# Kernel tuning notes

Hardware: AMD Instinct MI355X
Metric: run time of the kernel (lower is better)

## Reference

```python
import jax, jax.numpy as jnp
import numpy as np

P, M, DG, F, H, DH = 2000, 150, 2000, 256, 4, 64
N1, N2 = P + M, P + DG          # adj1 nodes (patient+med), adj2 nodes (patient+diag)
E1, E2, EGP, EGM = 137600, 256000, 64000, 4800
GNN_LAYERS = 2
SA_HID = 128


def setup_inputs() -> dict:
    key = jax.random.key(0)
    ks = jax.random.split(key, 32)
    ri = lambda k, n, hi: jax.random.randint(k, (n,), 0, hi, dtype=jnp.int32)
    rn = lambda k, shape, scale: (jax.random.normal(k, shape, dtype=jnp.float32) * scale)
    inp = {
        'adj1_rows': ri(ks[0], E1, N1), 'adj1_cols': ri(ks[1], E1, N1),
        'adj1_vals': jax.random.uniform(ks[2], (E1,), dtype=jnp.float32),
        'adj2_rows': ri(ks[3], E2, N2), 'adj2_cols': ri(ks[4], E2, N2),
        'adj2_vals': jax.random.uniform(ks[5], (E2,), dtype=jnp.float32),
        'g0_src': ri(ks[6], EGP, P), 'g0_dst': ri(ks[7], EGP, P),
        'g1_src': ri(ks[8], EGP, P), 'g1_dst': ri(ks[9], EGP, P),
        'g2_src': ri(ks[10], EGM, M), 'g2_dst': ri(ks[11], EGM, M),
        'g3_src': ri(ks[12], EGM, M), 'g3_dst': ri(ks[13], EGM, M),
        'keepRate': 1,
        # learned parameters (xavier-ish scales)
        'pEmbed': rn(ks[14], (P, F), 0.05),
        'mEmbed': rn(ks[15], (M, F), 0.05),
        'dEmbed': rn(ks[16], (DG, F), 0.05),
        'gat_W': rn(ks[17], (4, F, H * DH), (2.0 / (F + H * DH)) ** 0.5),
        'gat_al': rn(ks[18], (4, H, DH), 0.1),
        'gat_ar': rn(ks[19], (4, H, DH), 0.1),
        'gat_b': jnp.zeros((4, H * DH), dtype=jnp.float32),
        'sa_W1': rn(ks[20], (H * DH, SA_HID), (2.0 / (H * DH + SA_HID)) ** 0.5),
        'sa_b1': jnp.zeros((SA_HID,), dtype=jnp.float32),
        'sa_W2': rn(ks[21], (SA_HID, 1), 0.1),
        'out_W': rn(ks[22], (2 * F, M), (2.0 / (2 * F + M)) ** 0.5),
        'out_b': jnp.zeros((M,), dtype=jnp.float32),
    }
    return inp


def _spmm(rows, cols, vals, x, n):
    # sparse adj @ x via gather + segment_sum
    return jax.ops.segment_sum(vals[:, None] * x[cols], rows, num_segments=n)


def _seg_softmax(e, seg, n):
    m = jax.ops.segment_max(e, seg, num_segments=n)          # [n, H]
    ex = jnp.exp(e - m[seg])
    s = jax.ops.segment_sum(ex, seg, num_segments=n)
    return ex / (s[seg] + 1e-9)


def _gat(h, W, al, ar, b, src, dst, n):
    # DGL GATConv, feat/attn dropout = 0, negative_slope = 0.2, activation = elu
    feat = (h @ W).reshape(n, H, DH)                          # [n, H, DH]
    el = (feat * al[None]).sum(-1)                            # [n, H]
    er = (feat * ar[None]).sum(-1)
    e = jax.nn.leaky_relu(el[src] + er[dst], negative_slope=0.2)  # [E, H]
    alpha = _seg_softmax(e, dst, n)                           # softmax over in-edges per dst
    out = jax.ops.segment_sum(alpha[:, :, None] * feat[src], dst, num_segments=n)
    out = out + b.reshape(1, H, DH)
    return jax.nn.elu(out).reshape(n, H * DH)


def _sem_att(z, W1, b1, W2):
    # z: [N, K, F]; shared projection; beta over K meta-paths
    w = (jnp.tanh(z @ W1 + b1) @ W2).mean(0)                  # [K, 1]
    beta = jax.nn.softmax(w, axis=0)                          # [K, 1]
    return (beta[None] * z).sum(1)                            # [N, F]


def reference(adj1_rows, adj1_cols, adj1_vals, adj2_rows, adj2_cols, adj2_vals,
              g0_src, g0_dst, g1_src, g1_dst, g2_src, g2_dst, g3_src, g3_dst,
              keepRate, pEmbed, mEmbed, dEmbed, gat_W, gat_al, gat_ar, gat_b,
              sa_W1, sa_b1, sa_W2, out_W, out_b):
    embeds1 = jnp.concatenate([pEmbed, mEmbed], axis=0)       # [N1, F]
    embeds2 = jnp.concatenate([pEmbed, dEmbed], axis=0)       # [N2, F]
    lat1, lat2 = embeds1, embeds2
    acc1 = jnp.zeros_like(embeds1)
    acc2 = jnp.zeros_like(embeds2)
    for _ in range(GNN_LAYERS):
        lat1 = jax.nn.leaky_relu(_spmm(adj1_rows, adj1_cols, adj1_vals, lat1, N1), negative_slope=0.5)
        lat2 = jax.nn.leaky_relu(_spmm(adj2_rows, adj2_cols, adj2_vals, lat2, N2), negative_slope=0.5)
        acc1 = acc1 + lat1
        acc2 = acc2 + lat2
    p1, m_gcn = acc1[:P], acc1[P:]
    p2, d_gcn = acc2[:P], acc2[P:]

    e0 = _gat(p1, gat_W[0], gat_al[0], gat_ar[0], gat_b[0], g0_src, g0_dst, P)
    e1 = _gat(p2, gat_W[1], gat_al[1], gat_ar[1], gat_b[1], g1_src, g1_dst, P)
    e2 = _gat(m_gcn, gat_W[2], gat_al[2], gat_ar[2], gat_b[2], g2_src, g2_dst, M)
    e3 = _gat(m_gcn, gat_W[3], gat_al[3], gat_ar[3], gat_b[3], g3_src, g3_dst, M)

    patient = _sem_att(jnp.stack([e0, e1], axis=1), sa_W1, sa_b1, sa_W2)  # [P, F]
    med = _sem_att(jnp.stack([e2, e3], axis=1), sa_W1, sa_b1, sa_W2)      # [M, F]

    # broadcasted pairwise concat -> ReLU -> Linear -> sum over pairing axis
    pm = jnp.concatenate([
        jnp.broadcast_to(patient[:, None, :], (P, M, F)),
        jnp.broadcast_to(med[None, :, :], (P, M, F)),
    ], axis=-1).reshape(P * M, 2 * F)
    simi = (jax.nn.relu(pm) @ out_W + out_b).reshape(P, M, M)
    simi_pm = simi.sum(axis=1)                                # [P, M]
    return (simi_pm, d_gcn, med, m_gcn, patient)
```

## Files before the change

### kernel.cpp

```cpp
#include <hip/hip_runtime.h>
#include <hip/hip_fp16.h>
#include <cmath>
#include <cstdint>

constexpr int P  = 2000, M = 150, DG = 2000, F = 256, H = 4, DH = 64;
constexpr int N1 = P + M;
constexpr int N2 = P + DG;
constexpr int E1 = 137600, E2 = 256000, EGP = 64000, EGM = 4800;
constexpr int SA_HID = 128;

constexpr int HO1 = E1, HO2 = E1 + E2, HO3 = HO2 + EGP, HO4 = HO3 + EGP,
              HO5 = HO4 + EGM, HOE = HO5 + EGM;

constexpr int CAP_A = 160;
constexpr int CAP_G = 96;
constexpr int OVF_CAP = 4096;

constexpr int CPAD = 16;

__device__ __forceinline__ float4 h4_to_f4(const __half* p) {
  union { ushort4 u4; __half2 h2[2]; } u;
  u.u4 = *(const ushort4*)p;
  float2 lo = __half22float2(u.h2[0]);
  float2 hi = __half22float2(u.h2[1]);
  return make_float4(lo.x, lo.y, hi.x, hi.y);
}
__device__ __forceinline__ void f4_to_h4(__half* p, float4 v) {
  union { ushort4 u4; __half2 h2[2]; } u;
  u.h2[0] = __float22half2_rn(make_float2(v.x, v.y));
  u.h2[1] = __float22half2_rn(make_float2(v.z, v.w));
  *(ushort4*)p = u.u4;
}

constexpr int CAST_CH = (P * F + M * F + DG * F) / 8;

__global__ __launch_bounds__(256) void k_build(
    const int* __restrict__ a1r, const int* __restrict__ a1c, const float* __restrict__ a1v,
    const int* __restrict__ a2r, const int* __restrict__ a2c, const float* __restrict__ a2v,
    const int* __restrict__ d0, const int* __restrict__ s0,
    const int* __restrict__ d1, const int* __restrict__ s1,
    const int* __restrict__ d2, const int* __restrict__ s2,
    const int* __restrict__ d3, const int* __restrict__ s3,
    int* cur1, uint2* ell1, int* cur2, uint2* ell2,
    int* cu0, unsigned* eg0, int* cu1, unsigned* eg1,
    int* cu2, unsigned* eg2, int* cu3, unsigned* eg3,
    int* __restrict__ ovf_n, int4* __restrict__ ovf,
    const float* __restrict__ pEf, const float* __restrict__ mEf,
    const float* __restrict__ dEf,
    __half* __restrict__ pEh, __half* __restrict__ mEh, __half* __restrict__ dEh) {
  int tid = blockIdx.x * 256 + threadIdx.x;
  int T = gridDim.x * 256;
  int seg[4], row[4]; unsigned p0[4], p1[4];
#pragma unroll
  for (int u = 0; u < 4; ++u) {
    int i = tid + u * T;
    seg[u] = -1;
    if (i < HOE) {
      if (i < HO1)      { seg[u] = 0; row[u] = a1r[i]; p0[u] = (unsigned)a1c[i]; p1[u] = __float_as_uint(a1v[i]); }
      else if (i < HO2) { int j = i - HO1; seg[u] = 1; row[u] = a2r[j]; p0[u] = (unsigned)a2c[j]; p1[u] = __float_as_uint(a2v[j]); }
      else if (i < HO3) { int j = i - HO2; seg[u] = 2; row[u] = d0[j]; p0[u] = (unsigned)s0[j]; }
      else if (i < HO4) { int j = i - HO3; seg[u] = 3; row[u] = d1[j]; p0[u] = (unsigned)s1[j]; }
      else if (i < HO5) { int j = i - HO4; seg[u] = 4; row[u] = d2[j]; p0[u] = (unsigned)s2[j]; }
      else              { int j = i - HO5; seg[u] = 5; row[u] = d3[j]; p0[u] = (unsigned)s3[j]; }
    }
  }
#pragma unroll
  for (int u = 0; u < 4; ++u) {
    int r = row[u];
    switch (seg[u]) {
      case 0: { int slot = atomicAdd(&cur1[(size_t)r * CPAD], 1);
        if (slot < CAP_A) ell1[(size_t)r * CAP_A + slot] = make_uint2(p0[u], p1[u]);
        else { int o = atomicAdd(&ovf_n[0], 1); if (o < OVF_CAP) ovf[0 * OVF_CAP + o] = make_int4(r, (int)p0[u], (int)p1[u], 0); } } break;
      case 1: { int slot = atomicAdd(&cur2[(size_t)r * CPAD], 1);
        if (slot < CAP_A) ell2[(size_t)r * CAP_A + slot] = make_uint2(p0[u], p1[u]);
        else { int o = atomicAdd(&ovf_n[1], 1); if (o < OVF_CAP) ovf[1 * OVF_CAP + o] = make_int4(r, (int)p0[u], (int)p1[u], 0); } } break;
      case 2: { int slot = atomicAdd(&cu0[(size_t)r * CPAD], 1);
        if (slot < CAP_G) eg0[(size_t)r * CAP_G + slot] = p0[u];
        else { int o = atomicAdd(&ovf_n[2], 1); if (o < OVF_CAP) ovf[2 * OVF_CAP + o] = make_int4(r, (int)p0[u], 0, 0); } } break;
      case 3: { int slot = atomicAdd(&cu1[(size_t)r * CPAD], 1);
        if (slot < CAP_G) eg1[(size_t)r * CAP_G + slot] = p0[u];
        else { int o = atomicAdd(&ovf_n[3], 1); if (o < OVF_CAP) ovf[3 * OVF_CAP + o] = make_int4(r, (int)p0[u], 0, 0); } } break;
      case 4: { int slot = atomicAdd(&cu2[(size_t)r * CPAD], 1);
        if (slot < CAP_G) eg2[(size_t)r * CAP_G + slot] = p0[u];
        else { int o = atomicAdd(&ovf_n[4], 1); if (o < OVF_CAP) ovf[4 * OVF_CAP + o] = make_int4(r, (int)p0[u], 0, 0); } } break;
      case 5: { int slot = atomicAdd(&cu3[(size_t)r * CPAD], 1);
        if (slot < CAP_G) eg3[(size_t)r * CAP_G + slot] = p0[u];
        else { int o = atomicAdd(&ovf_n[5], 1); if (o < OVF_CAP) ovf[5 * OVF_CAP + o] = make_int4(r, (int)p0[u], 0, 0); } } break;
      default: break;
    }
  }
  for (int c = tid; c < CAST_CH; c += T) {
    int j = c * 8;
    const float* src; __half* dst;
    if (j < P * F)              { src = pEf + j;               dst = pEh + j; }
    else if (j < P * F + M * F) { src = mEf + (j - P * F);     dst = mEh + (j - P * F); }
    else                        { src = dEf + (j - P*F - M*F); dst = dEh + (j - P*F - M*F); }
    float4 a = *(const float4*)src, b = *(const float4*)(src + 4);
    f4_to_h4(dst, a);
    f4_to_h4(dst + 4, b);
  }
}

template<int LAYER>
__global__ __launch_bounds__(256) void k_spmm(
    const int* __restrict__ cur1, const uint2* __restrict__ ell1,
    const int* __restrict__ cur2, const uint2* __restrict__ ell2,
    const int* __restrict__ ovf_n, const int4* __restrict__ ovf,
    const __half* __restrict__ pEh, const __half* __restrict__ mEh,
    const __half* __restrict__ dEh,
    float* __restrict__ lat1f, float* __restrict__ lat2f,
    __half* __restrict__ lat1h, __half* __restrict__ lat2h,
    float* __restrict__ acc1, float* __restrict__ acc2,
    float* __restrict__ out_mgcn, float* __restrict__ out_dgcn) {
  int grp = (blockIdx.x * 256 + threadIdx.x) >> 7;
  int lane = threadIdx.x & 63;
  int wh   = (threadIdx.x >> 6) & 1;
  int gl   = threadIdx.x >> 7;
  bool g2 = grp >= N1;
  int row = g2 ? grp - N1 : grp;
  const uint2* pe = (g2 ? ell2 : ell1) + (size_t)row * CAP_A;
  const __half* latinh = g2 ? lat2h : lat1h;
  const __half* tailEh = g2 ? dEh : mEh;
  int deg = (g2 ? cur2 : cur1)[(size_t)row * CPAD];
  int dn = deg < CAP_A ? deg : CAP_A;
  int fo = lane << 2;
  float4 s = {0.f, 0.f, 0.f, 0.f};
  auto fetch = [&](int c) -> float4 {
    const __half* b;
    if (LAYER == 1) b = (c < P) ? (pEh + (size_t)c * F) : (tailEh + (size_t)(c - P) * F);
    else            b = latinh + (size_t)c * F;
    return h4_to_f4(b + fo);
  };
// ... 26 lines not shown
  }
  {
    int gi = g2 ? 1 : 0;
    int on = ovf_n[gi];
    if (on > 0) {
      const int4* ol = ovf + gi * OVF_CAP;
      for (int k = 0; k < on; ++k) {
        int4 e = ol[k];
        if (e.x == row) {
          float v = __int_as_float(e.z);
          float4 a = fetch(e.y);
          s.x += v * a.x; s.y += v * a.y; s.z += v * a.z; s.w += v * a.w;
        }
      }
    }
  }
  float4 l;
  l.x = s.x > 0.f ? s.x : 0.5f * s.x;
  l.y = s.y > 0.f ? s.y : 0.5f * s.y;
  l.z = s.z > 0.f ? s.z : 0.5f * s.z;
  l.w = s.w > 0.f ? s.w : 0.5f * s.w;
  if (LAYER == 1) {
    *(float4*)((g2 ? lat2f : lat1f) + (size_t)row * F + fo) = l;
    f4_to_h4((g2 ? lat2h : lat1h) + (size_t)row * F + fo, l);
  } else {
    const float* latf = g2 ? lat2f : lat1f;
    float4 b = *(const float4*)(latf + (size_t)row * F + fo);
    float4 a = {b.x + l.x, b.y + l.y, b.z + l.z, b.w + l.w};
    *(float4*)((g2 ? acc2 : acc1) + (size_t)row * F + fo) = a;
    if (row >= P)
      *(float4*)((g2 ? out_dgcn : out_mgcn) + (size_t)(row - P) * F + fo) = a;
  }
}

constexpr int FR  = 8;
constexpr int NB0 = (P + FR - 1) / FR;
constexpr int NB2 = (M + FR - 1) / FR;
constexpr int FEAT_BLOCKS = 2 * NB0 + 2 * NB2;

__global__ __launch_bounds__(256) void k_gat_feat_all(
    const float* __restrict__ acc1, const float* __restrict__ acc2,
    const float* __restrict__ gat_W, const float* __restrict__ gat_al,
    const float* __restrict__ gat_ar,
    __half* __restrict__ f0, __half* __restrict__ f1,
    __half* __restrict__ f2, __half* __restrict__ f3,
    float* __restrict__ el, float* __restrict__ er) {
  int b = blockIdx.x;
  int g, rb, n; const float* h; __half* fout;
  if (b < NB0)            { g = 0; rb = b;              n = P; h = acc1; fout = f0; }
  else if (b < 2 * NB0)   { g = 1; rb = b - NB0;        n = P; h = acc2; fout = f1; }
  else if (b < 2*NB0+NB2) { g = 2; rb = b - 2 * NB0;    n = M; h = acc1 + (size_t)P * F; fout = f2; }
  else                    { g = 3; rb = b - 2*NB0 - NB2; n = M; h = acc1 + (size_t)P * F; fout = f3; }
  int elo = (g == 0) ? 0 : (g == 1) ? P * H : (g == 2) ? 2 * P * H : (2 * P + M) * H;
  const float* W = gat_W + (size_t)g * F * F;
  __shared__ float hs[FR][F];
  int t = threadIdx.x;
  int r0 = rb * FR;
  for (int q = t; q < FR * 64; q += 256) {
    int r = q >> 6, ln = q & 63;
    int row = r0 + r;
    float4 v = {0.f, 0.f, 0.f, 0.f};
    if (row < n) v = *(const float4*)(h + (size_t)row * F + (ln << 2));
    *(float4*)&hs[r][ln << 2] = v;
  }
  __syncthreads();
  float acc[FR];
#pragma unroll
  for (int r = 0; r < FR; ++r) acc[r] = 0.f;
  for (int k = 0; k < F; k += 4) {
    float w0 = W[(size_t)k * F + t],       w1 = W[(size_t)(k + 1) * F + t],
          w2 = W[(size_t)(k + 2) * F + t], w3 = W[(size_t)(k + 3) * F + t];
// ... 107 lines not shown
  __shared__ float4 pacc[2][64];
  __shared__ float  pss[2][64];
  if (wh == 1) { pacc[gl][lane] = acc; pss[gl][lane] = ssum; }
  __syncthreads();
  if (wh == 1) return;
  {
    float4 pa = pacc[gl][lane];
    acc.x += pa.x; acc.y += pa.y; acc.z += pa.z; acc.w += pa.w;
    ssum += pss[gl][lane];
  }
  if (on > 0) {
    for (int k = 0; k < on; ++k) {
      int4 e = ol[k];
      if (e.x == row) {
        float a = elb[e.y * H + head] + erv; a = a > 0.f ? a : 0.2f * a;
        float x0 = expf(a - mx);
        float4 q0 = h4_to_f4(feat + (size_t)e.y * F + fo);
        ssum += x0;
        acc.x += x0 * q0.x; acc.y += x0 * q0.y; acc.z += x0 * q0.z; acc.w += x0 * q0.w;
      }
    }
  }
  float inv = 1.f / (ssum + 1e-9f);
  const float* bb = gat_b + g * F + fo;
  float4 v = {acc.x * inv + bb[0], acc.y * inv + bb[1],
              acc.z * inv + bb[2], acc.w * inv + bb[3]};
  v.x = v.x > 0.f ? v.x : expm1f(v.x);
  v.y = v.y > 0.f ? v.y : expm1f(v.y);
  v.z = v.z > 0.f ? v.z : expm1f(v.z);
  v.w = v.w > 0.f ? v.w : expm1f(v.w);
  *(float4*)(out + (size_t)row * F + fo) = v;
}

constexpr int SR  = 4;
constexpr int SB0 = (P + SR - 1) / SR;
constexpr int SB2 = (M + SR - 1) / SR;
constexpr int SEM_BLOCKS = 2 * SB0 + 2 * SB2;

__global__ __launch_bounds__(128) void k_sem_w_all(
    const float* __restrict__ e0, const float* __restrict__ e1,
    const float* __restrict__ e2, const float* __restrict__ e3,
    const float* __restrict__ W1, const float* __restrict__ b1,
    const float* __restrict__ W2, float* __restrict__ w) {
  int b = blockIdx.x;
  int zid, rb, n; const float* z;
  if (b < SB0)            { zid = 0; rb = b;             n = P; z = e0; }
  else if (b < 2 * SB0)   { zid = 1; rb = b - SB0;       n = P; z = e1; }
  else if (b < 2*SB0+SB2) { zid = 2; rb = b - 2 * SB0;   n = M; z = e2; }
  else                    { zid = 3; rb = b - 2*SB0-SB2; n = M; z = e3; }
  __shared__ float zs[SR][F];
  int t = threadIdx.x;
  int r0 = rb * SR;
  for (int q = t; q < SR * 64; q += 128) {
    int r = q >> 6, ln = q & 63;
    int row = r0 + r;
    float4 v = {0.f, 0.f, 0.f, 0.f};
    if (row < n) v = *(const float4*)(z + (size_t)row * F + (ln << 2));
    *(float4*)&zs[r][ln << 2] = v;
  }
  __syncthreads();
  float hid[SR];
#pragma unroll
  for (int r = 0; r < SR; ++r) hid[r] = b1[t];
  for (int k = 0; k < F; k += 4) {
    float w0 = W1[(size_t)k * SA_HID + t],       w1 = W1[(size_t)(k + 1) * SA_HID + t],
          w2 = W1[(size_t)(k + 2) * SA_HID + t], w3 = W1[(size_t)(k + 3) * SA_HID + t];
#pragma unroll
    for (int r = 0; r < SR; ++r) {
      float4 z4 = *(const float4*)&zs[r][k];
      hid[r] += z4.x * w0 + z4.y * w1 + z4.z * w2 + z4.w * w3;
    }
// ... 27 lines not shown
    float4 u0 = ((const float4*)e2)[j], u1 = ((const float4*)e3)[j];
    float4 r = {a0 * u0.x + a1 * u1.x, a0 * u0.y + a1 * u1.y,
                a0 * u0.z + a1 * u1.z, a0 * u0.w + a1 * u1.w};
    ((float4*)out_med)[j] = r;
    rs.x += r.x > 0.f ? r.x : 0.f;
    rs.y += r.y > 0.f ? r.y : 0.f;
    rs.z += r.z > 0.f ? r.z : 0.f;
    rs.w += r.w > 0.f ? r.w : 0.f;
  }
  __shared__ float4 sv4[4][64];
  sv4[t >> 6][t & 63] = rs;
  __syncthreads();
  __shared__ float sv[F];
  if (t < 64) {
    float4 a = sv4[0][t], b = sv4[1][t], c = sv4[2][t], d = sv4[3][t];
    sv[t * 4 + 0] = a.x + b.x + c.x + d.x;
    sv[t * 4 + 1] = a.y + b.y + c.y + d.y;
    sv[t * 4 + 2] = a.z + b.z + c.z + d.z;
    sv[t * 4 + 3] = a.w + b.w + c.w + d.w;
  }
  __syncthreads();
  if (t < M) {
    float cc = (float)M * outb[t];
    for (int f = 0; f < F; f += 4) {
      cc += sv[f]     * outW[(size_t)(F + f) * M + t]
          + sv[f + 1] * outW[(size_t)(F + f + 1) * M + t]
          + sv[f + 2] * outW[(size_t)(F + f + 2) * M + t]
          + sv[f + 3] * outW[(size_t)(F + f + 3) * M + t];
    }
    cbuf[t] = cc;
  }
}

constexpr int FIN_R = 4;
__global__ __launch_bounds__(256) void k_final(
    const float* __restrict__ e0, const float* __restrict__ e1,
    const float* __restrict__ w, const float* __restrict__ outW,
    const float* __restrict__ c,
    float* __restrict__ out_pat, float* __restrict__ simi) {
  float m0 = w[0] * (1.f / P), m1 = w[1] * (1.f / P);
  float mxv = fmaxf(m0, m1);
  float a0 = expf(m0 - mxv), a1 = expf(m1 - mxv);
  float sc = 1.f / (a0 + a1);
  a0 *= sc; a1 *= sc;
  __shared__ float psh[FIN_R][F];
  int t = threadIdx.x;
  int r0 = blockIdx.x * FIN_R;
  for (int q = t; q < FIN_R * 64; q += 256) {
    int r = q >> 6, ln = q & 63;
    size_t off = (size_t)(r0 + r) * F + (ln << 2);
    float4 u0 = *(const float4*)(e0 + off), u1 = *(const float4*)(e1 + off);
    float4 v = {a0 * u0.x + a1 * u1.x, a0 * u0.y + a1 * u1.y,
                a0 * u0.z + a1 * u1.z, a0 * u0.w + a1 * u1.w};
    *(float4*)(out_pat + off) = v;
    v.x = v.x > 0.f ? v.x : 0.f; v.y = v.y > 0.f ? v.y : 0.f;
    v.z = v.z > 0.f ? v.z : 0.f; v.w = v.w > 0.f ? v.w : 0.f;
    *(float4*)&psh[r][ln << 2] = v;
  }
  __syncthreads();
  if (t < M) {
    float acc[FIN_R];
#pragma unroll
    for (int r = 0; r < FIN_R; ++r) acc[r] = 0.f;
    for (int f = 0; f < F; f += 4) {
      float w0 = outW[(size_t)f * M + t],       w1 = outW[(size_t)(f + 1) * M + t],
            w2 = outW[(size_t)(f + 2) * M + t], w3 = outW[(size_t)(f + 3) * M + t];
#pragma unroll
// ... 17 lines not shown
  const int*   adj2_rows = (const int*)d_in[3];
  const int*   adj2_cols = (const int*)d_in[4];
  const float* adj2_vals = (const float*)d_in[5];
  const int*   g0_src = (const int*)d_in[6];
  const int*   g0_dst = (const int*)d_in[7];
  const int*   g1_src = (const int*)d_in[8];
  const int*   g1_dst = (const int*)d_in[9];
  const int*   g2_src = (const int*)d_in[10];
  const int*   g2_dst = (const int*)d_in[11];
  const int*   g3_src = (const int*)d_in[12];
  const int*   g3_dst = (const int*)d_in[13];
  const float* pE     = (const float*)d_in[15];
  const float* mE     = (const float*)d_in[16];
  const float* dE     = (const float*)d_in[17];
  const float* gat_W  = (const float*)d_in[18];
  const float* gat_al = (const float*)d_in[19];
  const float* gat_ar = (const float*)d_in[20];
  const float* gat_b  = (const float*)d_in[21];
  const float* sa_W1  = (const float*)d_in[22];
  const float* sa_b1  = (const float*)d_in[23];
  const float* sa_W2  = (const float*)d_in[24];
  const float* out_W  = (const float*)d_in[25];
  const float* out_b  = (const float*)d_in[26];

  int* ip = (int*)d_ws;
  int* cur1 = ip; ip += (size_t)N1 * CPAD;
  int* cur2 = ip; ip += (size_t)N2 * CPAD;
  int* cu0  = ip; ip += (size_t)P * CPAD;
  int* cu1  = ip; ip += (size_t)P * CPAD;
  int* cu2  = ip; ip += (size_t)M * CPAD;
  int* cu3  = ip; ip += (size_t)M * CPAD;
  int* ovf_n = ip; ip += 6;
  float* wbuf = (float*)ip; ip += 4;
  size_t memset_bytes = (size_t)((char*)ip - (char*)d_ws);

  uintptr_t up = ((uintptr_t)ip + 15) & ~(uintptr_t)15;
  int4* ovf = (int4*)up;
  uint2* ell1 = (uint2*)(ovf + 6 * OVF_CAP);
  uint2* ell2 = ell1 + (size_t)N1 * CAP_A;
  unsigned* eg0 = (unsigned*)(ell2 + (size_t)N2 * CAP_A);
  unsigned* eg1 = eg0 + (size_t)P * CAP_G;
  unsigned* eg2 = eg1 + (size_t)P * CAP_G;
  unsigned* eg3 = eg2 + (size_t)M * CAP_G;
  __half* hp = (__half*)(eg3 + (size_t)M * CAP_G);
  __half* pEh   = hp; hp += (size_t)P * F;
  __half* mEh   = hp; hp += (size_t)M * F;
  __half* dEh   = hp; hp += (size_t)DG * F;
  __half* lat1h = hp; hp += (size_t)N1 * F;
  __half* lat2h = hp; hp += (size_t)N2 * F;
  __half* f0h   = hp; hp += (size_t)P * F;
  __half* f1h   = hp; hp += (size_t)P * F;
  __half* f2h   = hp; hp += (size_t)M * F;
  __half* f3h   = hp; hp += (size_t)M * F;
  float* fp = (float*)hp;
  float* lat1f = fp; fp += (size_t)N1 * F;
  float* lat2f = fp; fp += (size_t)N2 * F;
  float* acc1  = fp; fp += (size_t)N1 * F;
  float* acc2  = fp; fp += (size_t)N2 * F;
  float* el    = fp; fp += (size_t)(2 * P + 2 * M) * H;
  float* er    = fp; fp += (size_t)(2 * P + 2 * M) * H;
  float* e0b   = fp; fp += (size_t)P * F;
  float* e1b   = fp; fp += (size_t)P * F;
  float* e2b   = fp; fp += (size_t)M * F;
  float* e3b   = fp; fp += (size_t)M * F;
  float* cbuf  = fp; fp += 256;

  float* out_simi = (float*)d_out;
  float* out_dgcn = out_simi + (size_t)P * M;
  float* out_med  = out_dgcn + (size_t)DG * F;
  float* out_mgcn = out_med  + (size_t)M * F;
  float* out_pat  = out_mgcn + (size_t)M * F;

  hipMemsetAsync(d_ws, 0, memset_bytes, stream);

  int eb = ((HOE + 3) / 4 + 255) / 256;
  k_build<<<eb, 256, 0, stream>>>(adj1_rows, adj1_cols, adj1_vals,
                                  adj2_rows, adj2_cols, adj2_vals,
                                  g0_dst, g0_src, g1_dst, g1_src,
                                  g2_dst, g2_src, g3_dst, g3_src,
                                  cur1, ell1, cur2, ell2,
                                  cu0, eg0, cu1, eg1, cu2, eg2, cu3, eg3,
                                  ovf_n, ovf,
                                  pE, mE, dE, pEh, mEh, dEh);

  int sb = (N1 + N2) / 2;
  k_spmm<1><<<sb, 256, 0, stream>>>(cur1, ell1, cur2, ell2, ovf_n, ovf,
                                    pEh, mEh, dEh, lat1f, lat2f, lat1h, lat2h,
                                    acc1, acc2, out_mgcn, out_dgcn);
  k_spmm<2><<<sb, 256, 0, stream>>>(cur1, ell1, cur2, ell2, ovf_n, ovf,
                                    pEh, mEh, dEh, lat1f, lat2f, lat1h, lat2h,
                                    acc1, acc2, out_mgcn, out_dgcn);

  k_gat_feat_all<<<FEAT_BLOCKS, 256, 0, stream>>>(acc1, acc2, gat_W, gat_al, gat_ar,
                                                  f0h, f1h, f2h, f3h, el, er);
  int ab = (2 * P + 2 * M) / 2;
  k_gat_agg_all<<<ab, 256, 0, stream>>>(cu0, eg0, cu1, eg1, cu2, eg2, cu3, eg3,
                                        ovf_n, ovf, el, er, f0h, f1h, f2h, f3h, gat_b,
                                        e0b, e1b, e2b, e3b);

  k_sem_w_all<<<SEM_BLOCKS, 128, 0, stream>>>(e0b, e1b, e2b, e3b, sa_W1, sa_b1, sa_W2, wbuf);

  k_med_cvec<<<1, 256, 0, stream>>>(e2b, e3b, wbuf, out_W, out_b, out_med, cbuf);

  k_final<<<P / FIN_R, 256, 0, stream>>>(e0b, e1b, wbuf, out_W, cbuf, out_pat, out_simi);
}
```

Baseline: 307.0 us.

## Fuse whole pipeline into one cooperative persistent kernel with grid syncs

Replaces the memset plus eight separate kernel launches with a single cooperative persistent kernel. Each stage runs as a grid-stride loop over the old block indices, separated by grid.sync. The workspace zeroing moves inside the kernel, and the single-block med/cvec stage is spread across the grid using atomics into a new svg buffer. This removes per-launch overhead and the serial single-block stage, at the cost of limited occupancy and grid barrier latency. The old launch path is kept as a fallback if the cooperative launch fails.

```diff
diff --git a/kernel.cpp b/kernel.cpp
--- a/kernel.cpp
+++ b/kernel.cpp
@@ -1,7 +1,10 @@
 #include <hip/hip_runtime.h>
+#include <hip/hip_cooperative_groups.h>
 #include <hip/hip_fp16.h>
 #include <cmath>
 #include <cstdint>
+
+namespace cg = cooperative_groups;
 
 constexpr int P  = 2000, M = 150, DG = 2000, F = 256, H = 4, DH = 64;
 constexpr int N1 = P + M;
@@ -33,6 +36,490 @@
 }
 
 constexpr int CAST_CH = (P * F + M * F + DG * F) / 8;
+
+constexpr int FR  = 8;
+constexpr int NB0 = (P + FR - 1) / FR;
+constexpr int NB2 = (M + FR - 1) / FR;
+constexpr int FEAT_BLOCKS = 2 * NB0 + 2 * NB2;
+
+constexpr int SR  = 4;
+constexpr int SB0 = (P + SR - 1) / SR;
+constexpr int SB2 = (M + SR - 1) / SR;
+constexpr int SEM_BLOCKS = 2 * SB0 + 2 * SB2;
+
+constexpr int FIN_R = 4;
+
+struct MegaArgs {
+  const int* a1r; const int* a1c; const float* a1v;
+  const int* a2r; const int* a2c; const float* a2v;
+  const int* g0s; const int* g0d; const int* g1s; const int* g1d;
+  const int* g2s; const int* g2d; const int* g3s; const int* g3d;
+  const float* pE; const float* mE; const float* dE;
+  const float* gat_W; const float* gat_al; const float* gat_ar; const float* gat_b;
+  const float* sa_W1; const float* sa_b1; const float* sa_W2;
+  const float* out_W; const float* out_b;
+  int* zbase; int zero_words;
+  int* cur1; int* cur2; int* cu0; int* cu1; int* cu2; int* cu3;
+  int* ovf_n; float* wbuf; float* svg;
+  int4* ovf; uint2* ell1; uint2* ell2;
+  unsigned* eg0; unsigned* eg1; unsigned* eg2; unsigned* eg3;
+  __half* pEh; __half* mEh; __half* dEh;
+  __half* lat1h; __half* lat2h;
+  __half* f0; __half* f1; __half* f2; __half* f3;
+  float* lat1f; float* lat2f; float* acc1; float* acc2;
+  float* el; float* er;
+  float* e0; float* e1; float* e2; float* e3;
+  float* out_simi; float* out_dgcn; float* out_med; float* out_mgcn; float* out_pat;
+};
+
+template<int LAYER>
+__device__ __forceinline__ void mega_spmm(const MegaArgs& aa, char* smem,
+                                          int tid, int bid, int nb) {
+  float* part = (float*)smem;
+  const int lane = tid & 63, wh = (tid >> 6) & 1, gl = tid >> 7;
+  const int fo = lane << 2;
+  for (int tb = bid; tb < (N1 + N2) / 2; tb += nb) {
+    const int grp = tb * 2 + gl;
+    const bool g2 = grp >= N1;
+    const int row = g2 ? grp - N1 : grp;
+    const uint2* pe = (g2 ? aa.ell2 : aa.ell1) + (size_t)row * CAP_A;
+    const __half* latinh = g2 ? aa.lat2h : aa.lat1h;
+    const __half* tailEh = g2 ? aa.dEh : aa.mEh;
+    int deg = (g2 ? aa.cur2 : aa.cur1)[(size_t)row * CPAD];
+    int dn = deg < CAP_A ? deg : CAP_A;
+    float4 s = {0.f, 0.f, 0.f, 0.f};
+    auto fetch = [&](int c) -> float4 {
+      const __half* b;
+      if (LAYER == 1) b = (c < P) ? (aa.pEh + (size_t)c * F) : (tailEh + (size_t)(c - P) * F);
+      else            b = latinh + (size_t)c * F;
+      return h4_to_f4(b + fo);
+    };
+    int i = wh;
+    for (; i + 15 <= dn; i += 16) {
+      uint2 m[8]; float4 q[8];
+#pragma unroll
+      for (int u = 0; u < 8; ++u) m[u] = pe[i + 2 * u];
+#pragma unroll
+      for (int u = 0; u < 8; ++u) q[u] = fetch((int)m[u].x);
+#pragma unroll
+      for (int u = 0; u < 8; ++u) {
+        float v = __uint_as_float(m[u].y);
+        s.x += v * q[u].x; s.y += v * q[u].y; s.z += v * q[u].z; s.w += v * q[u].w;
+      }
+    }
+    for (; i < dn; i += 2) {
+      uint2 m = pe[i];
+      float v = __uint_as_float(m.y);
+      float4 q = fetch((int)m.x);
+      s.x += v * q.x; s.y += v * q.y; s.z += v * q.z; s.w += v * q.w;
+    }
+    if (wh == 1) *(float4*)&part[gl * F + fo] = s;
+    __syncthreads();
+    if (wh == 0) {
+      float4 p = *(const float4*)&part[gl * F + fo];
+      s.x += p.x; s.y += p.y; s.z += p.z; s.w += p.w;
+      int gi = g2 ? 1 : 0;
+      int on = aa.ovf_n[gi];
+      if (on > 0) {
+        const int4* ol = aa.ovf + gi * OVF_CAP;
+        for (int k = 0; k < on; ++k) {
+          int4 e = ol[k];
+          if (e.x == row) {
+            float v = __int_as_float(e.z);
+            float4 q = fetch(e.y);
+            s.x += v * q.x; s.y += v * q.y; s.z += v * q.z; s.w += v * q.w;
+          }
+        }
+      }
+      float4 l;
+      l.x = s.x > 0.f ? s.x : 0.5f * s.x;
+      l.y = s.y > 0.f ? s.y : 0.5f * s.y;
+      l.z = s.z > 0.f ? s.z : 0.5f * s.z;
+      l.w = s.w > 0.f ? s.w : 0.5f * s.w;
+      if (LAYER == 1) {
+        *(float4*)((g2 ? aa.lat2f : aa.lat1f) + (size_t)row * F + fo) = l;
+        f4_to_h4((g2 ? aa.lat2h : aa.lat1h) + (size_t)row * F + fo, l);
+      } else {
+        const float* latf = g2 ? aa.lat2f : aa.lat1f;
+        float4 b = *(const float4*)(latf + (size_t)row * F + fo);
+        float4 o = {b.x + l.x, b.y + l.y, b.z + l.z, b.w + l.w};
+        *(float4*)((g2 ? aa.acc2 : aa.acc1) + (size_t)row * F + fo) = o;
+        if (row >= P)
+          *(float4*)((g2 ? aa.out_dgcn : aa.out_mgcn) + (size_t)(row - P) * F + fo) = o;
+      }
+    }
+    __syncthreads();
+  }
+}
+
+__device__ __forceinline__ void mega_feat(const MegaArgs& aa, char* smem,
+                                          int tid, int bid, int nb) {
+  float* hs = (float*)smem;
+  const int head = tid >> 6, d = tid & 63;
+  for (int b = bid; b < FEAT_BLOCKS; b += nb) {
+    int g, rb, n; const float* h; __half* fout;
+    if (b < NB0)              { g = 0; rb = b;                n = P; h = aa.acc1;                 fout = aa.f0; }
+    else if (b < 2 * NB0)     { g = 1; rb = b - NB0;          n = P; h = aa.acc2;                 fout = aa.f1; }
+    else if (b < 2*NB0+NB2)   { g = 2; rb = b - 2 * NB0;      n = M; h = aa.acc1 + (size_t)P * F; fout = aa.f2; }
+    else                      { g = 3; rb = b - 2*NB0 - NB2;  n = M; h = aa.acc1 + (size_t)P * F; fout = aa.f3; }
+    int elo = (g == 0) ? 0 : (g == 1) ? P * H : (g == 2) ? 2 * P * H : (2 * P + M) * H;
+    const float* W = aa.gat_W + (size_t)g * F * F;
+    int r0 = rb * FR;
+    for (int q = tid; q < FR * 64; q += 256) {
+      int r = q >> 6, ln = q & 63;
+      int row = r0 + r;
+      float4 v = {0.f, 0.f, 0.f, 0.f};
+      if (row < n) v = *(const float4*)(h + (size_t)row * F + (ln << 2));
+      *(float4*)&hs[r * F + (ln << 2)] = v;
+    }
+    __syncthreads();
+    float acc[FR];
+#pragma unroll
+    for (int r = 0; r < FR; ++r) acc[r] = 0.f;
+    for (int k = 0; k < F; k += 4) {
+      float w0 = W[(size_t)k * F + tid],       w1 = W[(size_t)(k + 1) * F + tid],
+            w2 = W[(size_t)(k + 2) * F + tid], w3 = W[(size_t)(k + 3) * F + tid];
+#pragma unroll
+      for (int r = 0; r < FR; ++r) {
+        float4 h4 = *(const float4*)&hs[r * F + k];
+        acc[r] += h4.x * w0 + h4.y * w1 + h4.z * w2 + h4.w * w3;
+      }
+    }
+    float av = aa.gat_al[g * H * DH + head * DH + d];
+    float rv = aa.gat_ar[g * H * DH + head * DH + d];
+#pragma unroll
+    for (int r = 0; r < FR; ++r) {
+      int row = r0 + r;
+      if (row < n) {
+        fout[(size_t)row * F + tid] = __float2half_rn(acc[r]);
+        float cl = acc[r] * av, cr = acc[r] * rv;
+        for (int o = 32; o > 0; o >>= 1) {
+          cl += __shfl_down(cl, o, 64);
+          cr += __shfl_down(cr, o, 64);
+        }
+        if (d == 0) { aa.el[elo + row * H + head] = cl; aa.er[elo + row * H + head] = cr; }
+      }
+    }
+    __syncthreads();
+  }
+}
+
+__device__ __forceinline__ void mega_agg(const MegaArgs& aa, char* smem,
+                                         int tid, int bid, int nb) {
+  float*  mxs  = (float*)smem;
+  float4* pacc = (float4*)(smem + 1024);
+  float*  pss  = (float*)(smem + 3072);
+  const int lane = tid & 63, wh = (tid >> 6) & 1, gl = tid >> 7;
+  const int head = lane >> 4, fo = lane << 2;
+  for (int tb = bid; tb < (2 * P + 2 * M) / 2; tb += nb) {
+    const int grp = tb * 2 + gl;
+    int g, row; const int* cu; const unsigned* eg; const __half* feat; float* out; int elo;
+    if (grp < P)            { g = 0; row = grp;             cu = aa.cu0; eg = aa.eg0; feat = aa.f0; out = aa.e0; elo = 0; }
+    else if (grp < 2 * P)   { g = 1; row = grp - P;         cu = aa.cu1; eg = aa.eg1; feat = aa.f1; out = aa.e1; elo = P * H; }
+    else if (grp < 2*P + M) { g = 2; row = grp - 2 * P;     cu = aa.cu2; eg = aa.eg2; feat = aa.f2; out = aa.e2; elo = 2 * P * H; }
+    else                    { g = 3; row = grp - 2 * P - M; cu = aa.cu3; eg = aa.eg3; feat = aa.f3; out = aa.e3; elo = (2 * P + M) * H; }
+    const float* elb = aa.el + elo;
+    float erv = aa.er[elo + row * H + head];
+    int deg = cu[(size_t)row * CPAD];
+    int dn = deg < CAP_G ? deg : CAP_G;
+    const unsigned* ps = eg + (size_t)row * CAP_G;
+    int on = aa.ovf_n[2 + g];
+    const int4* ol = aa.ovf + (2 + g) * OVF_CAP;
+    float mx = -3.4e38f;
+    int i = wh;
+    for (; i + 7 <= dn; i += 8) {
+      int s0 = (int)ps[i], s1 = (int)ps[i + 2], s2 = (int)ps[i + 4], s3 = (int)ps[i + 6];
+      float x = elb[s0 * H + head] + erv, y = elb[s1 * H + head] + erv,
+            z = elb[s2 * H + head] + erv, w = elb[s3 * H + head] + erv;
+      x = x > 0.f ? x : 0.2f * x; y = y > 0.f ? y : 0.2f * y;
+      z = z > 0.f ? z : 0.2f * z; w = w > 0.f ? w : 0.2f * w;
+      mx = fmaxf(mx, fmaxf(fmaxf(x, y), fmaxf(z, w)));
+    }
+    for (; i < dn; i += 2) {
+      float x = elb[(int)ps[i] * H + head] + erv;
+      x = x > 0.f ? x : 0.2f * x;
+      mx = fmaxf(mx, x);
+    }
+    if (wh == 0 && on > 0) {
+      for (int k = 0; k < on; ++k) {
+        int4 e = ol[k];
+        if (e.x == row) {
+          float x = elb[e.y * H + head] + erv;
+          x = x > 0.f ? x : 0.2f * x;
+          mx = fmaxf(mx, x);
+        }
+      }
+    }
+    mxs[(gl * 2 + wh) * 64 + lane] = mx;
+    __syncthreads();
+    mx = fmaxf(mxs[(gl * 2) * 64 + lane], mxs[(gl * 2 + 1) * 64 + lane]);
+    float ssum = 0.f;
+    float4 acc = {0.f, 0.f, 0.f, 0.f};
+    i = wh;
+    for (; i + 3 <= dn; i += 4) {
+      int s0 = (int)ps[i], s1 = (int)ps[i + 2];
+      float x = elb[s0 * H + head] + erv; x = x > 0.f ? x : 0.2f * x;
+      float y = elb[s1 * H + head] + erv; y = y > 0.f ? y : 0.2f * y;
+      float ex0 = expf(x - mx), ex1 = expf(y - mx);
+      float4 q0 = h4_to_f4(feat + (size_t)s0 * F + fo);
+      float4 q1 = h4_to_f4(feat + (size_t)s1 * F + fo);
+      ssum += ex0 + ex1;
+      acc.x += ex0 * q0.x + ex1 * q1.x;
+      acc.y += ex0 * q0.y + ex1 * q1.y;
+      acc.z += ex0 * q0.z + ex1 * q1.z;
+      acc.w += ex0 * q0.w + ex1 * q1.w;
+    }
+    for (; i < dn; i += 2) {
+      int s0 = (int)ps[i];
+      float x = elb[s0 * H + head] + erv; x = x > 0.f ? x : 0.2f * x;
+      float ex0 = expf(x - mx);
+      float4 q0 = h4_to_f4(feat + (size_t)s0 * F + fo);
+      ssum += ex0;
+      acc.x += ex0 * q0.x; acc.y += ex0 * q0.y; acc.z += ex0 * q0.z; acc.w += ex0 * q0.w;
+    }
+    if (wh == 1) { pacc[gl * 64 + lane] = acc; pss[gl * 64 + lane] = ssum; }
+    __syncthreads();
+    if (wh == 0) {
+      float4 pa = pacc[gl * 64 + lane];
+      acc.x += pa.x; acc.y += pa.y; acc.z += pa.z; acc.w += pa.w;
+      ssum += pss[gl * 64 + lane];
+      if (on > 0) {
+        for (int k = 0; k < on; ++k) {
+          int4 e = ol[k];
+          if (e.x == row) {
+            float x = elb[e.y * H + head] + erv; x = x > 0.f ? x : 0.2f * x;
+            float ex0 = expf(x - mx);
+            float4 q0 = h4_to_f4(feat + (size_t)e.y * F + fo);
+            ssum += ex0;
+            acc.x += ex0 * q0.x; acc.y += ex0 * q0.y; acc.z += ex0 * q0.z; acc.w += ex0 * q0.w;
+          }
+        }
+      }
+      float inv = 1.f / (ssum + 1e-9f);
+      const float* bb = aa.gat_b + g * F + fo;
+      float4 v = {acc.x * inv + bb[0], acc.y * inv + bb[1],
+                  acc.z * inv + bb[2], acc.w * inv + bb[3]};
+      v.x = v.x > 0.f ? v.x : expm1f(v.x);
+      v.y = v.y > 0.f ? v.y : expm1f(v.y);
+      v.z = v.z > 0.f ? v.z : expm1f(v.z);
+      v.w = v.w > 0.f ? v.w : expm1f(v.w);
+      *(float4*)(out + (size_t)row * F + fo) = v;
+    }
+    __syncthreads();
+  }
+}
+
+__device__ __forceinline__ void mega_sem(const MegaArgs& aa, char* smem,
+                                         int tid, int bid, int nb) {
+  float* zs = (float*)smem;
+  float* pp = (float*)(smem + 8192);
+  const int sub = tid >> 7, st = tid & 127;
+  for (int bt = bid; bt < SEM_BLOCKS / 2; bt += nb) {
+    int b = bt * 2 + sub;
+    int zid, rb, n; const float* z;
+    if (b < SB0)              { zid = 0; rb = b;               n = P; z = aa.e0; }
+    else if (b < 2 * SB0)     { zid = 1; rb = b - SB0;         n = P; z = aa.e1; }
+    else if (b < 2*SB0+SB2)   { zid = 2; rb = b - 2 * SB0;     n = M; z = aa.e2; }
+    else                      { zid = 3; rb = b - 2*SB0 - SB2; n = M; z = aa.e3; }
+    float* zsl = zs + sub * (SR * F);
+    int r0 = rb * SR;
+    for (int q = st; q < SR * 64; q += 128) {
+      int r = q >> 6, ln = q & 63;
+      int row = r0 + r;
+      float4 v = {0.f, 0.f, 0.f, 0.f};
+      if (row < n) v = *(const float4*)(z + (size_t)row * F + (ln << 2));
+      *(float4*)&zsl[r * F + (ln << 2)] = v;
+    }
+    __syncthreads();
+    float hid[SR];
+#pragma unroll
+    for (int r = 0; r < SR; ++r) hid[r] = aa.sa_b1[st];
+    for (int k = 0; k < F; k += 4) {
+      float w0 = aa.sa_W1[(size_t)k * SA_HID + st],       w1 = aa.sa_W1[(size_t)(k + 1) * SA_HID + st],
+            w2 = aa.sa_W1[(size_t)(k + 2) * SA_HID + st], w3 = aa.sa_W1[(size_t)(k + 3) * SA_HID + st];
+#pragma unroll
+      for (int r = 0; r < SR; ++r) {
+        float4 z4 = *(const float4*)&zsl[r * F + k];
+        hid[r] += z4.x * w0 + z4.y * w1 + z4.z * w2 + z4.w * w3;
+      }
+    }
+    float w2v = aa.sa_W2[st];
+    float local = 0.f;
+    for (int r = 0; r < SR; ++r) {
+      int row = r0 + r;
+      if (row < n) local += tanhf(hid[r]) * w2v;
+    }
+    for (int o = 32; o > 0; o >>= 1) local += __shfl_down(local, o, 64);
+    if ((st & 63) == 0) pp[sub * 2 + (st >> 6)] = local;
+    __syncthreads();
+    if (st == 0) atomicAdd(&aa.wbuf[zid], pp[sub * 2] + pp[sub * 2 + 1]);
+    __syncthreads();
+  }
+}
+
+__device__ __forceinline__ void mega_med(const MegaArgs& aa, char* smem,
+                                         int tid, int bid, int gtid, int gsz) {
+  constexpr int MED4 = M * F / 4;
+  float m0 = aa.wbuf[2] * (1.f / M), m1 = aa.wbuf[3] * (1.f / M);
+  float mxv = fmaxf(m0, m1);
+  float b0 = expf(m0 - mxv), b1 = expf(m1 - mxv);
+  float sc = 1.f / (b0 + b1);
+  b0 *= sc; b1 *= sc;
+  float4 rs = {0.f, 0.f, 0.f, 0.f};
+  for (int j = gtid; j < MED4; j += gsz) {
+    float4 u0 = ((const float4*)aa.e2)[j], u1 = ((const float4*)aa.e3)[j];
+    float4 r = {b0 * u0.x + b1 * u1.x, b0 * u0.y + b1 * u1.y,
+                b0 * u0.z + b1 * u1.z, b0 * u0.w + b1 * u1.w};
+    ((float4*)aa.out_med)[j] = r;
+    rs.x += r.x > 0.f ? r.x : 0.f;
+    rs.y += r.y > 0.f ? r.y : 0.f;
+    rs.z += r.z > 0.f ? r.z : 0.f;
+    rs.w += r.w > 0.f ? r.w : 0.f;
+  }
+  if (bid * 256 < MED4) {
+    float4* sv4 = (float4*)smem;
+    sv4[(tid >> 6) * 64 + (tid & 63)] = rs;
+    __syncthreads();
+    if (tid < 64) {
+      float4 x = sv4[tid], y = sv4[64 + tid], z = sv4[128 + tid], w = sv4[192 + tid];
+      atomicAdd(&aa.svg[tid * 4 + 0], x.x + y.x + z.x + w.x);
+      atomicAdd(&aa.svg[tid * 4 + 1], x.y + y.y + z.y + w.y);
+      atomicAdd(&aa.svg[tid * 4 + 2], x.z + y.z + z.z + w.z);
+      atomicAdd(&aa.svg[tid * 4 + 3], x.w + y.w + z.w + w.w);
+    }
+  }
+}
+
+__device__ __forceinline__ void mega_final(const MegaArgs& aa, char* smem,
+                                           int tid, int bid, int nb) {
+  float* svl = (float*)smem;
+  float* psh = (float*)(smem + 1024);
+  for (int q = tid; q < F; q += 256) svl[q] = aa.svg[q];
+  float m0 = aa.wbuf[0] * (1.f / P), m1 = aa.wbuf[1] * (1.f / P);
+  float mxv = fmaxf(m0, m1);
+  float b0 = expf(m0 - mxv), b1 = expf(m1 - mxv);
+  float sc = 1.f / (b0 + b1);
+  b0 *= sc; b1 *= sc;
+  __syncthreads();
+  float cv = 0.f;
+  if (tid < M) {
+    float cacc = 0.f;
+    for (int f = 0; f < F; f += 4) {
+      cacc += svl[f]     * aa.out_W[(size_t)(F + f)     * M + tid]
+            + svl[f + 1] * aa.out_W[(size_t)(F + f + 1) * M + tid]
+            + svl[f + 2] * aa.out_W[(size_t)(F + f + 2) * M + tid]
+            + svl[f + 3] * aa.out_W[(size_t)(F + f + 3) * M + tid];
+    }
+    cv = cacc + (float)M * aa.out_b[tid];
+  }
+  for (int bt = bid; bt < P / FIN_R; bt += nb) {
+    int r0 = bt * FIN_R;
+    for (int q = tid; q < FIN_R * 64; q += 256) {
+      int r = q >> 6, ln = q & 63;
+      size_t off = (size_t)(r0 + r) * F + (ln << 2);
+      float4 u0 = *(const float4*)(aa.e0 + off), u1 = *(const float4*)(aa.e1 + off);
+      float4 v = {b0 * u0.x + b1 * u1.x, b0 * u0.y + b1 * u1.y,
+                  b0 * u0.z + b1 * u1.z, b0 * u0.w + b1 * u1.w};
+      *(float4*)(aa.out_pat + off) = v;
+      v.x = v.x > 0.f ? v.x : 0.f; v.y = v.y > 0.f ? v.y : 0.f;
+      v.z = v.z > 0.f ? v.z : 0.f; v.w = v.w > 0.f ? v.w : 0.f;
+      *(float4*)&psh[r * F + (ln << 2)] = v;
+    }
+    __syncthreads();
+    if (tid < M) {
+      float acc[FIN_R];
+#pragma unroll
+      for (int r = 0; r < FIN_R; ++r) acc[r] = 0.f;
+      for (int f = 0; f < F; f += 4) {
+        float w0 = aa.out_W[(size_t)f * M + tid],       w1 = aa.out_W[(size_t)(f + 1) * M + tid],
+              w2 = aa.out_W[(size_t)(f + 2) * M + tid], w3 = aa.out_W[(size_t)(f + 3) * M + tid];
+#pragma unroll
+        for (int r = 0; r < FIN_R; ++r) {
+          float4 p4 = *(const float4*)&psh[r * F + f];
+          acc[r] += p4.x * w0 + p4.y * w1 + p4.z * w2 + p4.w * w3;
+        }
+      }
+#pragma unroll
+      for (int r = 0; r < FIN_R; ++r)
+        aa.out_simi[(size_t)(r0 + r) * M + tid] = (float)M * acc[r] + cv;
+    }
+    __syncthreads();
+  }
+}
+
+__global__ __launch_bounds__(256) void k_mega(MegaArgs aa) {
+  cg::grid_group grid = cg::this_grid();
+  const int tid = threadIdx.x, bid = blockIdx.x, nb = gridDim.x;
+  const int gtid = bid * 256 + tid, gsz = nb * 256;
+  __shared__ __align__(16) char smem[8448];
+
+  for (int i = gtid; i < aa.zero_words; i += gsz) aa.zbase[i] = 0;
+  grid.sync();
+
+  for (int i = gtid; i < HOE; i += gsz) {
+    if (i < HO1) {
+      int r = aa.a1r[i]; unsigned q0 = (unsigned)aa.a1c[i], q1 = __float_as_uint(aa.a1v[i]);
+      int slot = atomicAdd(&aa.cur1[(size_t)r * CPAD], 1);
+      if (slot < CAP_A) aa.ell1[(size_t)r * CAP_A + slot] = make_uint2(q0, q1);
+      else { int o = atomicAdd(&aa.ovf_n[0], 1); if (o < OVF_CAP) aa.ovf[0 * OVF_CAP + o] = make_int4(r, (int)q0, (int)q1, 0); }
+    } else if (i < HO2) {
+      int j = i - HO1;
+      int r = aa.a2r[j]; unsigned q0 = (unsigned)aa.a2c[j], q1 = __float_as_uint(aa.a2v[j]);
+      int slot = atomicAdd(&aa.cur2[(size_t)r * CPAD], 1);
+      if (slot < CAP_A) aa.ell2[(size_t)r * CAP_A + slot] = make_uint2(q0, q1);
+      else { int o = atomicAdd(&aa.ovf_n[1], 1); if (o < OVF_CAP) aa.ovf[1 * OVF_CAP + o] = make_int4(r, (int)q0, (int)q1, 0); }
+    } else if (i < HO3) {
+      int j = i - HO2;
+      int r = aa.g0d[j]; unsigned q0 = (unsigned)aa.g0s[j];
+      int slot = atomicAdd(&aa.cu0[(size_t)r * CPAD], 1);
+      if (slot < CAP_G) aa.eg0[(size_t)r * CAP_G + slot] = q0;
+      else { int o = atomicAdd(&aa.ovf_n[2], 1); if (o < OVF_CAP) aa.ovf[2 * OVF_CAP + o] = make_int4(r, (int)q0, 0, 0); }
+    } else if (i < HO4) {
+      int j = i - HO3;
+      int r = aa.g1d[j]; unsigned q0 = (unsigned)aa.g1s[j];
+      int slot = atomicAdd(&aa.cu1[(size_t)r * CPAD], 1);
+      if (slot < CAP_G) aa.eg1[(size_t)r * CAP_G + slot] = q0;
+      else { int o = atomicAdd(&aa.ovf_n[3], 1); if (o < OVF_CAP) aa.ovf[3 * OVF_CAP + o] = make_int4(r, (int)q0, 0, 0); }
+    } else if (i < HO5) {
+      int j = i - HO4;
+      int r = aa.g2d[j]; unsigned q0 = (unsigned)aa.g2s[j];
+      int slot = atomicAdd(&aa.cu2[(size_t)r * CPAD], 1);
+      if (slot < CAP_G) aa.eg2[(size_t)r * CAP_G + slot] = q0;
+      else { int o = atomicAdd(&aa.ovf_n[4], 1); if (o < OVF_CAP) aa.ovf[4 * OVF_CAP + o] = make_int4(r, (int)q0, 0, 0); }
+    } else {
+      int j = i - HO5;
+      int r = aa.g3d[j]; unsigned q0 = (unsigned)aa.g3s[j];
+      int slot = atomicAdd(&aa.cu3[(size_t)r * CPAD], 1);
+      if (slot < CAP_G) aa.eg3[(size_t)r * CAP_G + slot] = q0;
+      else { int o = atomicAdd(&aa.ovf_n[5], 1); if (o < OVF_CAP) aa.ovf[5 * OVF_CAP + o] = make_int4(r, (int)q0, 0, 0); }
+    }
+  }
+  for (int c = gtid; c < CAST_CH; c += gsz) {
+    int j = c * 8;
+    const float* src; __half* dst;
+    if (j < P * F)              { src = aa.pE + j;                 dst = aa.pEh + j; }
+    else if (j < P * F + M * F) { src = aa.mE + (j - P * F);       dst = aa.mEh + (j - P * F); }
+    else                        { src = aa.dE + (j - P*F - M*F);   dst = aa.dEh + (j - P*F - M*F); }
+    float4 x = *(const float4*)src, y = *(const float4*)(src + 4);
+    f4_to_h4(dst, x);
+    f4_to_h4(dst + 4, y);
+  }
+  grid.sync();
+
+  mega_spmm<1>(aa, smem, tid, bid, nb);
+  grid.sync();
+  mega_spmm<2>(aa, smem, tid, bid, nb);
+  grid.sync();
+  mega_feat(aa, smem, tid, bid, nb);
+  grid.sync();
+  mega_agg(aa, smem, tid, bid, nb);
+  grid.sync();
+  mega_sem(aa, smem, tid, bid, nb);
+  grid.sync();
+  mega_med(aa, smem, tid, bid, gtid, gsz);
+  grid.sync();
+  mega_final(aa, smem, tid, bid, nb);
+}
 
 __global__ __launch_bounds__(256) void k_build(
     const int* __restrict__ a1r, const int* __restrict__ a1c, const float* __restrict__ a1v,
@@ -95,9 +582,9 @@
     if (j < P * F)              { src = pEf + j;               dst = pEh + j; }
     else if (j < P * F + M * F) { src = mEf + (j - P * F);     dst = mEh + (j - P * F); }
     else                        { src = dEf + (j - P*F - M*F); dst = dEh + (j - P*F - M*F); }
-    float4 a = *(const float4*)src, b = *(const float4*)(src + 4);
-    f4_to_h4(dst, a);
-    f4_to_h4(dst + 4, b);
+    float4 x = *(const float4*)src, y = *(const float4*)(src + 4);
+    f4_to_h4(dst, x);
+    f4_to_h4(dst + 4, y);
   }
 }
 
@@ -190,11 +677,6 @@
       *(float4*)((g2 ? out_dgcn : out_mgcn) + (size_t)(row - P) * F + fo) = a;
   }
 }
-
-constexpr int FR  = 8;
-constexpr int NB0 = (P + FR - 1) / FR;
-constexpr int NB2 = (M + FR - 1) / FR;
-constexpr int FEAT_BLOCKS = 2 * NB0 + 2 * NB2;
 
 __global__ __launch_bounds__(256) void k_gat_feat_all(
     const float* __restrict__ acc1, const float* __restrict__ acc2,
@@ -368,11 +850,6 @@
   *(float4*)(out + (size_t)row * F + fo) = v;
 }
 
-constexpr int SR  = 4;
-constexpr int SB0 = (P + SR - 1) / SR;
-constexpr int SB2 = (M + SR - 1) / SR;
-constexpr int SEM_BLOCKS = 2 * SB0 + 2 * SB2;
-
 __global__ __launch_bounds__(128) void k_sem_w_all(
     const float* __restrict__ e0, const float* __restrict__ e1,
     const float* __restrict__ e2, const float* __restrict__ e3,
@@ -466,7 +943,6 @@
   }
 }
 
-constexpr int FIN_R = 4;
 __global__ __launch_bounds__(256) void k_final(
     const float* __restrict__ e0, const float* __restrict__ e1,
     const float* __restrict__ w, const float* __restrict__ outW,
@@ -550,7 +1026,9 @@
   int* cu3  = ip; ip += (size_t)M * CPAD;
   int* ovf_n = ip; ip += 6;
   float* wbuf = (float*)ip; ip += 4;
-  size_t memset_bytes = (size_t)((char*)ip - (char*)d_ws);
+  float* svg  = (float*)ip; ip += F;
+  int zero_words = (int)(ip - (int*)d_ws);
+  size_t memset_bytes = (size_t)zero_words * 4;
 
   uintptr_t up = ((uintptr_t)ip + 15) & ~(uintptr_t)15;
   int4* ovf = (int4*)up;
@@ -589,36 +1067,73 @@
   float* out_mgcn = out_med  + (size_t)M * F;
   float* out_pat  = out_mgcn + (size_t)M * F;
 
-  hipMemsetAsync(d_ws, 0, memset_bytes, stream);
-
-  int eb = ((HOE + 3) / 4 + 255) / 256;
-  k_build<<<eb, 256, 0, stream>>>(adj1_rows, adj1_cols, adj1_vals,
-                                  adj2_rows, adj2_cols, adj2_vals,
-                                  g0_dst, g0_src, g1_dst, g1_src,
-                                  g2_dst, g2_src, g3_dst, g3_src,
-                                  cur1, ell1, cur2, ell2,
-                                  cu0, eg0, cu1, eg1, cu2, eg2, cu3, eg3,
-                                  ovf_n, ovf,
-                                  pE, mE, dE, pEh, mEh, dEh);
-
-  int sb = (N1 + N2) / 2;
-  k_spmm<1><<<sb, 256, 0, stream>>>(cur1, ell1, cur2, ell2, ovf_n, ovf,
-                                    pEh, mEh, dEh, lat1f, lat2f, lat1h, lat2h,
-                                    acc1, acc2, out_mgcn, out_dgcn);
-  k_spmm<2><<<sb, 256, 0, stream>>>(cur1, ell1, cur2, ell2, ovf_n, ovf,
-                                    pEh, mEh, dEh, lat1f, lat2f, lat1h, lat2h,
-                                    acc1, acc2, out_mgcn, out_dgcn);
-
-  k_gat_feat_all<<<FEAT_BLOCKS, 256, 0, stream>>>(acc1, acc2, gat_W, gat_al, gat_ar,
-                                                  f0h, f1h, f2h, f3h, el, er);
-  int ab = (2 * P + 2 * M) / 2;
-  k_gat_agg_all<<<ab, 256, 0, stream>>>(cu0, eg0, cu1, eg1, cu2, eg2, cu3, eg3,
-                                        ovf_n, ovf, el, er, f0h, f1h, f2h, f3h, gat_b,
-                                        e0b, e1b, e2b, e3b);
-
-  k_sem_w_all<<<SEM_BLOCKS, 128, 0, stream>>>(e0b, e1b, e2b, e3b, sa_W1, sa_b1, sa_W2, wbuf);
-
-  k_med_cvec<<<1, 256, 0, stream>>>(e2b, e3b, wbuf, out_W, out_b, out_med, cbuf);
-
-  k_final<<<P / FIN_R, 256, 0, stream>>>(e0b, e1b, wbuf, out_W, cbuf, out_pat, out_simi);
-}
+  static int  s_grid = 0;
+  static bool s_coop = true;
+  if (s_grid == 0) {
+    int nbk = 0;
+    if (hipOccupancyMaxActiveBlocksPerMultiprocessor(&nbk, k_mega, 256, 0) != hipSuccess || nbk < 1)
+      nbk = 1;
+    long g = (long)nbk * 256;
+    if (g > 3072) g = 3072;
+    s_grid = (int)g;
+  }
+  bool done = false;
+  if (s_coop) {
+    MegaArgs ma;
+    ma.a1r = adj1_rows; ma.a1c = adj1_cols; ma.a1v = adj1_vals;
+    ma.a2r = adj2_rows; ma.a2c = adj2_cols; ma.a2v = adj2_vals;
+    ma.g0s = g0_src; ma.g0d = g0_dst; ma.g1s = g1_src; ma.g1d = g1_dst;
+    ma.g2s = g2_src; ma.g2d = g2_dst; ma.g3s = g3_src; ma.g3d = g3_dst;
+    ma.pE = pE; ma.mE = mE; ma.dE = dE;
+    ma.gat_W = gat_W; ma.gat_al = gat_al; ma.gat_ar = gat_ar; ma.gat_b = gat_b;
+    ma.sa_W1 = sa_W1; ma.sa_b1 = sa_b1; ma.sa_W2 = sa_W2;
+    ma.out_W = out_W; ma.out_b = out_b;
+    ma.zbase = (int*)d_ws; ma.zero_words = zero_words;
+    ma.cur1 = cur1; ma.cur2 = cur2; ma.cu0 = cu0; ma.cu1 = cu1; ma.cu2 = cu2; ma.cu3 = cu3;
+    ma.ovf_n = ovf_n; ma.wbuf = wbuf; ma.svg = svg;
+    ma.ovf = ovf; ma.ell1 = ell1; ma.ell2 = ell2;
+    ma.eg0 = eg0; ma.eg1 = eg1; ma.eg2 = eg2; ma.eg3 = eg3;
+    ma.pEh = pEh; ma.mEh = mEh; ma.dEh = dEh;
+    ma.lat1h = lat1h; ma.lat2h = lat2h;
+    ma.f0 = f0h; ma.f1 = f1h; ma.f2 = f2h; ma.f3 = f3h;
+    ma.lat1f = lat1f; ma.lat2f = lat2f; ma.acc1 = acc1; ma.acc2 = acc2;
+    ma.el = el; ma.er = er;
+    ma.e0 = e0b; ma.e1 = e1b; ma.e2 = e2b; ma.e3 = e3b;
+    ma.out_simi = out_simi; ma.out_dgcn = out_dgcn; ma.out_med = out_med;
+    ma.out_mgcn = out_mgcn; ma.out_pat = out_pat;
+    void* kargs[] = { &ma };
+    hipError_t e = hipLaunchCooperativeKernel((const void*)k_mega, dim3(s_grid),
+                                              dim3(256), kargs, 0, stream);
+    if (e == hipSuccess) done = true;
+    else s_coop = false;
+  }
+
+  if (!done) {
+    hipMemsetAsync(d_ws, 0, memset_bytes, stream);
+    int eb = ((HOE + 3) / 4 + 255) / 256;
+    k_build<<<eb, 256, 0, stream>>>(adj1_rows, adj1_cols, adj1_vals,
+                                    adj2_rows, adj2_cols, adj2_vals,
+                                    g0_dst, g0_src, g1_dst, g1_src,
+                                    g2_dst, g2_src, g3_dst, g3_src,
+                                    cur1, ell1, cur2, ell2,
+                                    cu0, eg0, cu1, eg1, cu2, eg2, cu3, eg3,
+                                    ovf_n, ovf,
+                                    pE, mE, dE, pEh, mEh, dEh);
+    int sb = (N1 + N2) / 2;
+    k_spmm<1><<<sb, 256, 0, stream>>>(cur1, ell1, cur2, ell2, ovf_n, ovf,
+                                      pEh, mEh, dEh, lat1f, lat2f, lat1h, lat2h,
+                                      acc1, acc2, out_mgcn, out_dgcn);
+    k_spmm<2><<<sb, 256, 0, stream>>>(cur1, ell1, cur2, ell2, ovf_n, ovf,
+                                      pEh, mEh, dEh, lat1f, lat2f, lat1h, lat2h,
+                                      acc1, acc2, out_mgcn, out_dgcn);
+    k_gat_feat_all<<<FEAT_BLOCKS, 256, 0, stream>>>(acc1, acc2, gat_W, gat_al, gat_ar,
+                                                    f0h, f1h, f2h, f3h, el, er);
+    int ab = (2 * P + 2 * M) / 2;
+    k_gat_agg_all<<<ab, 256, 0, stream>>>(cu0, eg0, cu1, eg1, cu2, eg2, cu3, eg3,
+                                          ovf_n, ovf, el, er, f0h, f1h, f2h, f3h, gat_b,
+                                          e0b, e1b, e2b, e3b);
+    k_sem_w_all<<<SEM_BLOCKS, 128, 0, stream>>>(e0b, e1b, e2b, e3b, sa_W1, sa_b1, sa_W2, wbuf);
+    k_med_cvec<<<1, 256, 0, stream>>>(e2b, e3b, wbuf, out_W, out_b, out_med, cbuf);
+    k_final<<<P / FIN_R, 256, 0, stream>>>(e0b, e1b, wbuf, out_W, cbuf, out_pat, out_simi);
+  }
+}
```

Measured after the change: 843.2 us. +174.6%, slower.
